# Optimization experiments

Measured on AMD Instinct MI355X. Metric: run time of the kernel, lower is better.

Reference implementation:

```python
import jax, jax.numpy as jnp
import numpy as np

B, N, DIM = 4, 4096, 1024
HEADS, DIM_HEAD = 16, 64
ATTN_SCALE = 8.0
EPS = 1e-12


def setup_inputs() -> dict:
    key = jax.random.key(0)
    k1, k2, k3 = jax.random.split(key, 3)
    dim_inner = HEADS * DIM_HEAD
    return {
        "x": jax.random.normal(k1, (B, N, DIM), dtype=jnp.float32),
        "gamma": jnp.ones((DIM,), dtype=jnp.float32),
        "w_qkv": jax.random.normal(k2, (3 * dim_inner, DIM), dtype=jnp.float32) * 0.02,
        "temperature": jnp.ones((HEADS, 1, 1), dtype=jnp.float32),
        "w_out": jax.random.normal(k3, (DIM, dim_inner), dtype=jnp.float32) * 0.02,
    }


def _l2norm(t, axis=-1):
    # matches F.normalize: x / max(||x||, eps)
    n = jnp.sqrt(jnp.sum(t * t, axis=axis, keepdims=True))
    return t / jnp.maximum(n, EPS)


def reference(x, gamma, w_qkv, temperature, w_out):
    b, n, dim = x.shape
    h, dh = HEADS, DIM_HEAD
    # RMSNorm: F.normalize(x, dim=-1) * sqrt(dim) * gamma
    xn = _l2norm(x) * jnp.sqrt(jnp.float32(dim)) * gamma
    # QKV projection, rearrange 'b n (qkv h d) -> qkv b h d n'
    qkv = jnp.einsum('bnc,oc->bno', xn, w_qkv)
    qkv = qkv.reshape(b, n, 3, h, dh).transpose(2, 0, 3, 4, 1)  # (3, b, h, dh, n)
    q, k, v = qkv[0], qkv[1], qkv[2]
    # l2-normalize along n (last axis), learned per-head temperature on q
    q = _l2norm(q) * jnp.exp(temperature)
    k = _l2norm(k)
    # cross-covariance attention over feature dim: scores are (b,h,dh,dh)
    sim = jnp.einsum('bhdn,bhen->bhde', q, k) * ATTN_SCALE
    attn = jax.nn.softmax(sim, axis=-1)
    out = jnp.einsum('bhde,bhen->bhdn', attn, v)
    # rearrange 'b h d n -> b n (h d)' and output projection
    out = out.transpose(0, 3, 1, 2).reshape(b, n, h * dh)
    return jnp.einsum('bni,oi->bno', out, w_out)
```

## Files before the change

### kernel.cpp

```cpp
#include <hip/hip_runtime.h>
#include <hip/hip_bf16.h>
#include <cstdint>
#include <cstddef>

#define BB    4
#define NN    4096
#define DIM   1024
#define HEADS 16
#define DH    64
#define DIN   1024
#define NQO   3072
#define MTOT  (BB*NN)
#define KDIM  1024
#define EPS_F 1e-12f

using bf16 = __hip_bfloat16;
typedef __attribute__((ext_vector_type(8))) short bf16x8;
typedef __attribute__((ext_vector_type(4))) float f32x4;

__device__ __forceinline__ void gload_lds16(const void* g, void* l) {
    __builtin_amdgcn_global_load_lds(
        (const __attribute__((address_space(1))) void*)g,
        (__attribute__((address_space(3))) void*)l,
        16, 0, 0);
}

__device__ __forceinline__ ushort bf16_bits(float x) {
    union { bf16 h; ushort u; } c;
    c.h = __float2bfloat16(x);
    return c.u;
}

__device__ __forceinline__ float b2f(ushort u) {
    union { unsigned u32; float f; } c;
    c.u32 = ((unsigned)u) << 16;
    return c.f;
}

__global__ __launch_bounds__(256) void k_rmsnorm(const float* __restrict__ x,
                                                 const float* __restrict__ gamma,
                                                 bf16* __restrict__ xn) {
    int row = blockIdx.x;
    int t = threadIdx.x;
    const float4* xr = (const float4*)(x + (size_t)row * DIM);
    float4 v = xr[t];
    float ss = v.x * v.x + v.y * v.y + v.z * v.z + v.w * v.w;
#pragma unroll
    for (int off = 32; off; off >>= 1) ss += __shfl_down(ss, off, 64);
    __shared__ float red[4];
    int lane = t & 63, w = t >> 6;
    if (lane == 0) red[w] = ss;
    __syncthreads();
    float tot = red[0] + red[1] + red[2] + red[3];
    float scale = 32.0f / fmaxf(sqrtf(tot), EPS_F);
    float4 g = ((const float4*)gamma)[t];
    union { ushort4 u4; ushort us[4]; } o;
    o.us[0] = bf16_bits(v.x * scale * g.x);
    o.us[1] = bf16_bits(v.y * scale * g.y);
    o.us[2] = bf16_bits(v.z * scale * g.z);
    o.us[3] = bf16_bits(v.w * scale * g.w);
    ((ushort4*)(xn + (size_t)row * DIM))[t] = o.u4;
}

__global__ __launch_bounds__(256) void k_cast_bf16(const float* __restrict__ s,
                                                   bf16* __restrict__ d, int n4) {
    int i = blockIdx.x * blockDim.x + threadIdx.x;
    if (i >= n4) return;
    float4 v = ((const float4*)s)[i];
    union { ushort4 u4; ushort us[4]; } o;
    o.us[0] = bf16_bits(v.x); o.us[1] = bf16_bits(v.y);
    o.us[2] = bf16_bits(v.z); o.us[3] = bf16_bits(v.w);
    ((ushort4*)d)[i] = o.u4;
}

__global__ __launch_bounds__(256, 2) void k_gemm_qkv(const bf16* __restrict__ A,
                                                     const bf16* __restrict__ W,
                                                     bf16* __restrict__ qkv) {
    __shared__ short As[128 * 32];
    __shared__ short Bs[128 * 32];
    const int tm = blockIdx.y * 128;
    const int tn = blockIdx.x * 128;
    const int t = threadIdx.x, lane = t & 63, w = t >> 6;
    const int wr = w >> 1, wc = w & 1;

    f32x4 acc[4][4] = {};

    const int ca = w * 2;
    const int rowS = ca * 16 + (lane >> 2);
    const int kofs = (lane & 3) * 8;
    const bf16* Ab = A + (size_t)(tm + rowS) * KDIM + kofs;
    const bf16* Bb = W + (size_t)(tn + rowS) * KDIM + kofs;
    short* AsD0 = As + ca * 512;
    short* AsD1 = As + (ca + 1) * 512;
    short* BsD0 = Bs + ca * 512;
    short* BsD1 = Bs + (ca + 1) * 512;

    const int rbA = wr * 64 + (lane & 15);
    const int rbB = wc * 64 + (lane & 15);
    const int kh = (lane >> 4) * 8;

    for (int kk = 0; kk < KDIM; kk += 32) {
        __syncthreads();
        gload_lds16(Ab + kk, AsD0);
        gload_lds16(Ab + kk + 16 * KDIM, AsD1);
        gload_lds16(Bb + kk, BsD0);
        gload_lds16(Bb + kk + 16 * KDIM, BsD1);
        __syncthreads();
        bf16x8 af[4], bfr[4];
#pragma unroll
        for (int i = 0; i < 4; ++i) {
            af[i]  = *(const bf16x8*)(As + (rbA + i * 16) * 32 + kh);
            bfr[i] = *(const bf16x8*)(Bs + (rbB + i * 16) * 32 + kh);
        }
#pragma unroll
        for (int i = 0; i < 4; ++i)
#pragma unroll
            for (int j = 0; j < 4; ++j)
                acc[i][j] = __builtin_amdgcn_mfma_f32_16x16x32_bf16(af[i], bfr[j], acc[i][j], 0, 0, 0);
    }

    const int b = tm >> 12;
#pragma unroll
    for (int i = 0; i < 4; ++i) {
        int mg = tm + wr * 64 + i * 16 + (lane >> 4) * 4;
        int nseq = mg & (NN - 1);
#pragma unroll
        for (int j = 0; j < 4; ++j) {
            int o = tn + wc * 64 + j * 16 + (lane & 15);
            size_t row = (size_t)((o >> 10) * 4 + b) * 1024 + (o & 1023);
            union { ushort4 u4; ushort us[4]; } pk;
#pragma unroll
            for (int r = 0; r < 4; ++r) pk.us[r] = bf16_bits(acc[i][j][r]);
            *(ushort4*)(qkv + row * NN + nseq) = pk.u4;
        }
    }
}

__global__ __launch_bounds__(256) void k_rownorm(const bf16* __restrict__ qkv,
                                                 float* __restrict__ inv) {
    int row = blockIdx.x;
    const short* p = (const short*)(qkv + (size_t)row * NN);
    int t = threadIdx.x;
    bf16x8 a = *(const bf16x8*)(p + t * 16);
    bf16x8 b = *(const bf16x8*)(p + t * 16 + 8);
    float ss = 0.f;
#pragma unroll
    for (int i = 0; i < 8; ++i) {
        float fa = b2f((ushort)a[i]), fb = b2f((ushort)b[i]);
        ss += fa * fa + fb * fb;
    }
#pragma unroll
    for (int off = 32; off; off >>= 1) ss += __shfl_down(ss, off, 64);
    __shared__ float red[4];
    int lane = t & 63, w = t >> 6;
    if (lane == 0) red[w] = ss;
    __syncthreads();
    if (t == 0) {
        float tot = red[0] + red[1] + red[2] + red[3];
        inv[row] = 1.0f / fmaxf(sqrtf(tot), EPS_F);
    }
}

__global__ __launch_bounds__(256) void k_sim(const bf16* __restrict__ qkv,
                                             float* __restrict__ part) {
    __shared__ short Qs[64 * 32];
    __shared__ short Ks[64 * 32];
    const int chunk = blockIdx.x;
    const int bh = blockIdx.y;
    const int t = threadIdx.x, lane = t & 63, w = t >> 6;
    const bf16* qb = qkv + (size_t)(bh * 64) * NN;
    const bf16* kb = qkv + (size_t)(4096 + bh * 64) * NN;

    const size_t gofs = (size_t)(t >> 2) * NN + (t & 3) * 8 + chunk * 1024;
    short* QsD = Qs + w * 512;
    short* KsD = Ks + w * 512;

    const int ra = (w * 16 + (lane & 15)) * 32 + (lane >> 4) * 8;
    const int kh = (lane >> 4) * 8;

    f32x4 acc[4] = {};
    for (int nt = 0; nt < 32; ++nt) {
        __syncthreads();
        gload_lds16(qb + gofs + nt * 32, QsD);
        gload_lds16(kb + gofs + nt * 32, KsD);
        __syncthreads();
        bf16x8 af = *(const bf16x8*)(Qs + ra);
#pragma unroll
        for (int j = 0; j < 4; ++j) {
            bf16x8 bfr = *(const bf16x8*)(Ks + (j * 16 + (lane & 15)) * 32 + kh);
            acc[j] = __builtin_amdgcn_mfma_f32_16x16x32_bf16(af, bfr, acc[j], 0, 0, 0);
        }
    }
    float* pb = part + (size_t)(bh * 4 + chunk) * 4096;
#pragma unroll
    for (int j = 0; j < 4; ++j) {
        int e = j * 16 + (lane & 15);
#pragma unroll
        for (int r = 0; r < 4; ++r) {
            int d = w * 16 + (lane >> 4) * 4 + r;
            pb[d * 64 + e] = acc[j][r];
        }
    }
}

__global__ __launch_bounds__(256) void k_softfin(const float* __restrict__ part,
                                                 const float* __restrict__ inv,
                                                 const float* __restrict__ temp,
                                                 float* __restrict__ attnT) {
    int bh = blockIdx.x;
    int t = threadIdx.x, lane = t & 63, w = t >> 6;
    int e = lane;
    float expT = __expf(temp[bh & (HEADS - 1)]);
    float ike = inv[4096 + bh * 64 + e] * 8.0f * expT;
    const float* pb = part + (size_t)bh * 4 * 4096;
#pragma unroll 4
    for (int dd = 0; dd < 16; ++dd) {
        int d = w * 16 + dd;
        float s = pb[d * 64 + e] + pb[4096 + d * 64 + e] +
                  pb[8192 + d * 64 + e] + pb[12288 + d * 64 + e];
        float logit = s * ike * inv[bh * 64 + d];
        float m = logit;
#pragma unroll
        for (int off = 32; off; off >>= 1) m = fmaxf(m, __shfl_xor(m, off, 64));
        float p = __expf(logit - m);
        float sum = p;
#pragma unroll
        for (int off = 32; off; off >>= 1) sum += __shfl_xor(sum, off, 64);
        attnT[(size_t)bh * 4096 + e * 64 + d] = p / sum;
    }
}

__global__ __launch_bounds__(256) void k_attnv(const bf16* __restrict__ qkv,
                                               const float* __restrict__ attnT,
                                               bf16* __restrict__ A2) {
    int nchunk = blockIdx.x;
    int bh = blockIdx.y;
    int dz = blockIdx.z;
    int t = threadIdx.x;
    int n = nchunk * 1024 + t * 4;
    const bf16* vb = qkv + (size_t)(8192 + bh * 64) * NN;
    const float* at = attnT + (size_t)bh * 4096 + dz * 32;
    float acc[32][4];
#pragma unroll
    for (int d = 0; d < 32; ++d)
#pragma unroll
        for (int r = 0; r < 4; ++r) acc[d][r] = 0.f;

    for (int e = 0; e < 64; ++e) {
        ushort4 vraw = *(const ushort4*)((const short*)vb + (size_t)e * NN + n);
        float v0 = b2f(vraw.x), v1 = b2f(vraw.y), v2 = b2f(vraw.z), v3 = b2f(vraw.w);
        const float* arow = at + e * 64;
#pragma unroll
        for (int d = 0; d < 32; ++d) {
            float a = arow[d];
            acc[d][0] = fmaf(a, v0, acc[d][0]);
            acc[d][1] = fmaf(a, v1, acc[d][1]);
            acc[d][2] = fmaf(a, v2, acc[d][2]);
            acc[d][3] = fmaf(a, v3, acc[d][3]);
        }
    }
    int b = bh >> 4, h = bh & 15;
#pragma unroll
    for (int r = 0; r < 4; ++r) {
        bf16* dst = A2 + (size_t)(b * NN + n + r) * DIN + h * 64 + dz * 32;
        alignas(16) ushort tmp[32];
#pragma unroll
        for (int d = 0; d < 32; ++d) tmp[d] = bf16_bits(acc[d][r]);
        uint4* d4 = (uint4*)dst;
        const uint4* s4 = (const uint4*)tmp;
        d4[0] = s4[0]; d4[1] = s4[1]; d4[2] = s4[2]; d4[3] = s4[3];
    }
}

__global__ __launch_bounds__(256, 2) void k_gemm_out(const bf16* __restrict__ A,
                                                     const bf16* __restrict__ W,
                                                     float* __restrict__ out) {
    __shared__ short As[128 * 32];
    __shared__ short Bs[128 * 32];
    const int tm = blockIdx.y * 128;
    const int tn = blockIdx.x * 128;
    const int t = threadIdx.x, lane = t & 63, w = t >> 6;
    const int wr = w >> 1, wc = w & 1;

    f32x4 acc[4][4] = {};

    const int ca = w * 2;
    const int rowS = ca * 16 + (lane >> 2);
    const int kofs = (lane & 3) * 8;
    const bf16* Ab = A + (size_t)(tm + rowS) * KDIM + kofs;
    const bf16* Bb = W + (size_t)(tn + rowS) * KDIM + kofs;
    short* AsD0 = As + ca * 512;
    short* AsD1 = As + (ca + 1) * 512;
    short* BsD0 = Bs + ca * 512;
    short* BsD1 = Bs + (ca + 1) * 512;

    const int rbA = wr * 64 + (lane & 15);
    const int rbB = wc * 64 + (lane & 15);
    const int kh = (lane >> 4) * 8;

    for (int kk = 0; kk < KDIM; kk += 32) {
        __syncthreads();
        gload_lds16(Ab + kk, AsD0);
        gload_lds16(Ab + kk + 16 * KDIM, AsD1);
        gload_lds16(Bb + kk, BsD0);
        gload_lds16(Bb + kk + 16 * KDIM, BsD1);
        __syncthreads();
        bf16x8 af[4], bfr[4];
#pragma unroll
        for (int i = 0; i < 4; ++i) {
            af[i]  = *(const bf16x8*)(As + (rbA + i * 16) * 32 + kh);
            bfr[i] = *(const bf16x8*)(Bs + (rbB + i * 16) * 32 + kh);
        }
#pragma unroll
        for (int i = 0; i < 4; ++i)
#pragma unroll
            for (int j = 0; j < 4; ++j)
                acc[i][j] = __builtin_amdgcn_mfma_f32_16x16x32_bf16(af[i], bfr[j], acc[i][j], 0, 0, 0);
    }

#pragma unroll
    for (int i = 0; i < 4; ++i) {
        int mg = tm + wr * 64 + i * 16 + (lane >> 4) * 4;
#pragma unroll
        for (int j = 0; j < 4; ++j) {
            int o = tn + wc * 64 + j * 16 + (lane & 15);
#pragma unroll
            for (int r = 0; r < 4; ++r)
                out[(size_t)(mg + r) * DIN + o] = acc[i][j][r];
        }
    }
}

extern "C" void kernel_launch(void* const* d_in, const int* in_sizes, int n_in,
                              void* d_out, int out_size, void* d_ws, size_t ws_size,
                              hipStream_t stream) {
    const float* x      = (const float*)d_in[0];
    const float* gamma  = (const float*)d_in[1];
    const float* w_qkv  = (const float*)d_in[2];
    const float* temp   = (const float*)d_in[3];
    const float* w_out  = (const float*)d_in[4];
    float* out = (float*)d_out;

    char* ws = (char*)d_ws;
    bf16*  qkv   = (bf16*)ws;
    bf16*  xn    = (bf16*)(ws + 100663296);
    bf16*  wq_bf = (bf16*)(ws + 134217728);
    bf16*  wo_bf = (bf16*)(ws + 140509184);
    float* inv   = (float*)(ws + 142606336);
    float* part  = (float*)(ws + 142639104);
    float* attnT = (float*)(ws + 146833408);

    k_rmsnorm<<<MTOT, 256, 0, stream>>>(x, gamma, xn);
    k_cast_bf16<<<(NQO * KDIM / 4 + 255) / 256, 256, 0, stream>>>(w_qkv, wq_bf, NQO * KDIM / 4);
    k_cast_bf16<<<(DIN * KDIM / 4 + 255) / 256, 256, 0, stream>>>(w_out, wo_bf, DIN * KDIM / 4);
    k_gemm_qkv<<<dim3(NQO / 128, MTOT / 128), 256, 0, stream>>>(xn, wq_bf, qkv);
    k_rownorm<<<8192, 256, 0, stream>>>(qkv, inv);
    k_sim<<<dim3(4, 64), 256, 0, stream>>>(qkv, part);
    k_softfin<<<64, 256, 0, stream>>>(part, inv, temp, attnT);
    bf16* A2 = xn;
    k_attnv<<<dim3(4, 64, 2), 256, 0, stream>>>(qkv, attnT, A2);
    k_gemm_out<<<dim3(DIN / 128, MTOT / 128), 256, 0, stream>>>(A2, wo_bf, out);
}
```

Measured before the change: 388.2 us.

## Fuse row norms into sim kernel and move attn@V onto MFMA with transposed V

Removes the separate row-norm kernel by accumulating q/k sum-of-squares inside the sim kernel via atomics, with a zeroing kernel added first. The sim kernel gets double-buffered swizzled LDS staging for K and doubles the chunk count. The QKV GEMM writes V in an (n, d) transposed layout so the attn@V step can run on bf16 MFMA, replacing the scalar FMA loop. Softmax weights are now stored as bf16 rather than fp32. In exchange, the transposed V stores are scattered 2-byte writes, the atomics add contention, and bf16 attention weights lose precision.

```diff
diff --git a/kernel.cpp b/kernel.cpp
--- a/kernel.cpp
+++ b/kernel.cpp
@@ -73,6 +73,11 @@
     ((ushort4*)d)[i] = o.u4;
 }
 
+__global__ __launch_bounds__(256) void k_zero(float* __restrict__ p, int n) {
+    int i = blockIdx.x * 256 + threadIdx.x;
+    if (i < n) p[i] = 0.0f;
+}
+
 __global__ __launch_bounds__(256, 2) void k_gemm_qkv(const bf16* __restrict__ A,
                                                      const bf16* __restrict__ W,
                                                      bf16* __restrict__ qkv) {
@@ -120,105 +125,133 @@
     }
 
     const int b = tm >> 12;
-#pragma unroll
-    for (int i = 0; i < 4; ++i) {
-        int mg = tm + wr * 64 + i * 16 + (lane >> 4) * 4;
-        int nseq = mg & (NN - 1);
-#pragma unroll
-        for (int j = 0; j < 4; ++j) {
-            int o = tn + wc * 64 + j * 16 + (lane & 15);
-            size_t row = (size_t)((o >> 10) * 4 + b) * 1024 + (o & 1023);
-            union { ushort4 u4; ushort us[4]; } pk;
-#pragma unroll
-            for (int r = 0; r < 4; ++r) pk.us[r] = bf16_bits(acc[i][j][r]);
-            *(ushort4*)(qkv + row * NN + nseq) = pk.u4;
-        }
-    }
-}
-
-__global__ __launch_bounds__(256) void k_rownorm(const bf16* __restrict__ qkv,
-                                                 float* __restrict__ inv) {
-    int row = blockIdx.x;
-    const short* p = (const short*)(qkv + (size_t)row * NN);
-    int t = threadIdx.x;
-    bf16x8 a = *(const bf16x8*)(p + t * 16);
-    bf16x8 b = *(const bf16x8*)(p + t * 16 + 8);
-    float ss = 0.f;
-#pragma unroll
-    for (int i = 0; i < 8; ++i) {
-        float fa = b2f((ushort)a[i]), fb = b2f((ushort)b[i]);
-        ss += fa * fa + fb * fb;
-    }
-#pragma unroll
-    for (int off = 32; off; off >>= 1) ss += __shfl_down(ss, off, 64);
-    __shared__ float red[4];
-    int lane = t & 63, w = t >> 6;
-    if (lane == 0) red[w] = ss;
-    __syncthreads();
-    if (t == 0) {
-        float tot = red[0] + red[1] + red[2] + red[3];
-        inv[row] = 1.0f / fmaxf(sqrtf(tot), EPS_F);
+    if (tn < 2048) {
+#pragma unroll
+        for (int i = 0; i < 4; ++i) {
+            int mg = tm + wr * 64 + i * 16 + ((lane >> 4) << 2);
+            int nseq = mg & (NN - 1);
+#pragma unroll
+            for (int j = 0; j < 4; ++j) {
+                int o = tn + wc * 64 + j * 16 + (lane & 15);
+                size_t row = (size_t)((o >> 10) * 4 + b) * 1024 + (o & 1023);
+                union { ushort4 u4; ushort us[4]; } pk;
+#pragma unroll
+                for (int r = 0; r < 4; ++r) pk.us[r] = bf16_bits(acc[i][j][r]);
+                *(ushort4*)(qkv + row * NN + nseq) = pk.u4;
+            }
+        }
+    } else {
+        bf16* vT = qkv + (size_t)8192 * NN;
+#pragma unroll
+        for (int i = 0; i < 4; ++i) {
+            int mg = tm + wr * 64 + i * 16 + ((lane >> 4) << 2);
+            int nseq = mg & (NN - 1);
+#pragma unroll
+            for (int j = 0; j < 4; ++j) {
+                int o = tn + wc * 64 + j * 16 + (lane & 15);
+                int hd = o & 1023;
+                size_t base = ((size_t)(b * 16 + (hd >> 6)) * NN + nseq) * 64 + (hd & 63);
+#pragma unroll
+                for (int r = 0; r < 4; ++r)
+                    vT[base + (size_t)r * 64] = __float2bfloat16(acc[i][j][r]);
+            }
+        }
     }
 }
 
 __global__ __launch_bounds__(256) void k_sim(const bf16* __restrict__ qkv,
-                                             float* __restrict__ part) {
-    __shared__ short Qs[64 * 32];
-    __shared__ short Ks[64 * 32];
+                                             float* __restrict__ part,
+                                             float* __restrict__ ss) {
+    __shared__ short Ks[2][8192];
     const int chunk = blockIdx.x;
     const int bh = blockIdx.y;
     const int t = threadIdx.x, lane = t & 63, w = t >> 6;
     const bf16* qb = qkv + (size_t)(bh * 64) * NN;
     const bf16* kb = qkv + (size_t)(4096 + bh * 64) * NN;
-
-    const size_t gofs = (size_t)(t >> 2) * NN + (t & 3) * 8 + chunk * 1024;
-    short* QsD = Qs + w * 512;
-    short* KsD = Ks + w * 512;
-
-    const int ra = (w * 16 + (lane & 15)) * 32 + (lane >> 4) * 8;
-    const int kh = (lane >> 4) * 8;
+    const int n0b = chunk * 512;
+
+#define SIM_STAGE(buf, nt) do {                                              \
+    int n0_ = n0b + (nt) * 128;                                              \
+    _Pragma("unroll")                                                        \
+    for (int cc = 0; cc < 4; ++cc) {                                         \
+        int row_ = cc * 16 + (t >> 4);                                       \
+        int colb_ = ((t & 15) << 4) ^ ((row_ & 7) << 4);                     \
+        gload_lds16(kb + (size_t)row_ * NN + n0_ + (colb_ >> 1),             \
+                    &Ks[buf][cc * 2048 + w * 512]);                          \
+    }                                                                        \
+} while (0)
 
     f32x4 acc[4] = {};
-    for (int nt = 0; nt < 32; ++nt) {
-        __syncthreads();
-        gload_lds16(qb + gofs + nt * 32, QsD);
-        gload_lds16(kb + gofs + nt * 32, KsD);
-        __syncthreads();
-        bf16x8 af = *(const bf16x8*)(Qs + ra);
-#pragma unroll
-        for (int j = 0; j < 4; ++j) {
-            bf16x8 bfr = *(const bf16x8*)(Ks + (j * 16 + (lane & 15)) * 32 + kh);
-            acc[j] = __builtin_amdgcn_mfma_f32_16x16x32_bf16(af, bfr, acc[j], 0, 0, 0);
-        }
-    }
-    float* pb = part + (size_t)(bh * 4 + chunk) * 4096;
+    float ssq = 0.f, ssk = 0.f;
+
+    SIM_STAGE(0, 0);
+    __syncthreads();
+    for (int nt = 0; nt < 4; ++nt) {
+        if (nt < 3) SIM_STAGE((nt + 1) & 1, nt + 1);
+        {
+            const int buf = nt & 1;
+            const int n0 = n0b + nt * 128;
+            bf16x8 af[4];
+#pragma unroll
+            for (int ks = 0; ks < 4; ++ks) {
+                af[ks] = *(const bf16x8*)(qb + (size_t)(w * 16 + (lane & 15)) * NN +
+                                          n0 + ks * 32 + ((lane >> 4) << 3));
+#pragma unroll
+                for (int i = 0; i < 8; ++i) { float f = b2f((ushort)af[ks][i]); ssq += f * f; }
+            }
+#pragma unroll
+            for (int j = 0; j < 4; ++j) {
+                int e = j * 16 + (lane & 15);
+#pragma unroll
+                for (int ks = 0; ks < 4; ++ks) {
+                    bf16x8 bfr = *(const bf16x8*)((const char*)&Ks[buf][0] + e * 256 +
+                                  ((ks * 64 + ((lane >> 4) << 4)) ^ ((e & 7) << 4)));
+                    if (j == w) {
+#pragma unroll
+                        for (int i = 0; i < 8; ++i) { float f = b2f((ushort)bfr[i]); ssk += f * f; }
+                    }
+                    acc[j] = __builtin_amdgcn_mfma_f32_16x16x32_bf16(af[ks], bfr, acc[j], 0, 0, 0);
+                }
+            }
+        }
+        __syncthreads();
+    }
+#undef SIM_STAGE
+
+    float vq = ssq; vq += __shfl_xor(vq, 16, 64); vq += __shfl_xor(vq, 32, 64);
+    if (lane < 16) atomicAdd(&ss[bh * 64 + w * 16 + lane], vq);
+    float vk = ssk; vk += __shfl_xor(vk, 16, 64); vk += __shfl_xor(vk, 32, 64);
+    if (lane < 16) atomicAdd(&ss[4096 + bh * 64 + w * 16 + lane], vk);
+
+    float* pb = part + (size_t)(bh * 8 + chunk) * 4096;
 #pragma unroll
     for (int j = 0; j < 4; ++j) {
         int e = j * 16 + (lane & 15);
 #pragma unroll
         for (int r = 0; r < 4; ++r) {
-            int d = w * 16 + (lane >> 4) * 4 + r;
+            int d = w * 16 + ((lane >> 4) << 2) + r;
             pb[d * 64 + e] = acc[j][r];
         }
     }
 }
 
 __global__ __launch_bounds__(256) void k_softfin(const float* __restrict__ part,
-                                                 const float* __restrict__ inv,
+                                                 const float* __restrict__ ss,
                                                  const float* __restrict__ temp,
-                                                 float* __restrict__ attnT) {
+                                                 bf16* __restrict__ attn) {
     int bh = blockIdx.x;
-    int t = threadIdx.x, lane = t & 63, w = t >> 6;
-    int e = lane;
+    int t = threadIdx.x, e = t & 63, w = t >> 6;
     float expT = __expf(temp[bh & (HEADS - 1)]);
-    float ike = inv[4096 + bh * 64 + e] * 8.0f * expT;
-    const float* pb = part + (size_t)bh * 4 * 4096;
-#pragma unroll 4
+    float ike = 8.0f * expT / fmaxf(sqrtf(ss[4096 + bh * 64 + e]), EPS_F);
+    const float* pb = part + (size_t)bh * 8 * 4096;
+#pragma unroll 2
     for (int dd = 0; dd < 16; ++dd) {
         int d = w * 16 + dd;
-        float s = pb[d * 64 + e] + pb[4096 + d * 64 + e] +
-                  pb[8192 + d * 64 + e] + pb[12288 + d * 64 + e];
-        float logit = s * ike * inv[bh * 64 + d];
+        float s = 0.f;
+#pragma unroll
+        for (int c = 0; c < 8; ++c) s += pb[c * 4096 + d * 64 + e];
+        float invq = 1.0f / fmaxf(sqrtf(ss[bh * 64 + d]), EPS_F);
+        float logit = s * ike * invq;
         float m = logit;
 #pragma unroll
         for (int off = 32; off; off >>= 1) m = fmaxf(m, __shfl_xor(m, off, 64));
@@ -226,50 +259,51 @@
         float sum = p;
 #pragma unroll
         for (int off = 32; off; off >>= 1) sum += __shfl_xor(sum, off, 64);
-        attnT[(size_t)bh * 4096 + e * 64 + d] = p / sum;
+        attn[(size_t)bh * 4096 + d * 64 + e] = __float2bfloat16(p / sum);
     }
 }
 
 __global__ __launch_bounds__(256) void k_attnv(const bf16* __restrict__ qkv,
-                                               const float* __restrict__ attnT,
+                                               const bf16* __restrict__ attn,
                                                bf16* __restrict__ A2) {
-    int nchunk = blockIdx.x;
-    int bh = blockIdx.y;
-    int dz = blockIdx.z;
-    int t = threadIdx.x;
-    int n = nchunk * 1024 + t * 4;
-    const bf16* vb = qkv + (size_t)(8192 + bh * 64) * NN;
-    const float* at = attnT + (size_t)bh * 4096 + dz * 32;
-    float acc[32][4];
-#pragma unroll
-    for (int d = 0; d < 32; ++d)
-#pragma unroll
-        for (int r = 0; r < 4; ++r) acc[d][r] = 0.f;
-
-    for (int e = 0; e < 64; ++e) {
-        ushort4 vraw = *(const ushort4*)((const short*)vb + (size_t)e * NN + n);
-        float v0 = b2f(vraw.x), v1 = b2f(vraw.y), v2 = b2f(vraw.z), v3 = b2f(vraw.w);
-        const float* arow = at + e * 64;
-#pragma unroll
-        for (int d = 0; d < 32; ++d) {
-            float a = arow[d];
-            acc[d][0] = fmaf(a, v0, acc[d][0]);
-            acc[d][1] = fmaf(a, v1, acc[d][1]);
-            acc[d][2] = fmaf(a, v2, acc[d][2]);
-            acc[d][3] = fmaf(a, v3, acc[d][3]);
-        }
-    }
-    int b = bh >> 4, h = bh & 15;
-#pragma unroll
-    for (int r = 0; r < 4; ++r) {
-        bf16* dst = A2 + (size_t)(b * NN + n + r) * DIN + h * 64 + dz * 32;
-        alignas(16) ushort tmp[32];
-#pragma unroll
-        for (int d = 0; d < 32; ++d) tmp[d] = bf16_bits(acc[d][r]);
-        uint4* d4 = (uint4*)dst;
-        const uint4* s4 = (const uint4*)tmp;
-        d4[0] = s4[0]; d4[1] = s4[1]; d4[2] = s4[2]; d4[3] = s4[3];
-    }
+    const int nc = blockIdx.x;
+    const int bh = blockIdx.y;
+    const int t = threadIdx.x, lane = t & 63, w = t >> 6;
+    const bf16* vT = qkv + (size_t)8192 * NN + (size_t)bh * NN * 64;
+    const bf16* ab = attn + (size_t)bh * 4096;
+    const int nbase = nc * 256 + w * 64;
+
+    bf16x8 bfr[4][2];
+#pragma unroll
+    for (int df = 0; df < 4; ++df)
+#pragma unroll
+        for (int ks = 0; ks < 2; ++ks)
+            bfr[df][ks] = *(const bf16x8*)(ab + (df * 16 + (lane & 15)) * 64 +
+                                           ks * 32 + ((lane >> 4) << 3));
+
+    f32x4 acc[4][4] = {};
+#pragma unroll
+    for (int nf = 0; nf < 4; ++nf) {
+#pragma unroll
+        for (int ks = 0; ks < 2; ++ks) {
+            bf16x8 af = *(const bf16x8*)(vT + (size_t)(nbase + nf * 16 + (lane & 15)) * 64 +
+                                         ks * 32 + ((lane >> 4) << 3));
+#pragma unroll
+            for (int df = 0; df < 4; ++df)
+                acc[nf][df] = __builtin_amdgcn_mfma_f32_16x16x32_bf16(af, bfr[df][ks], acc[nf][df], 0, 0, 0);
+        }
+    }
+    const int b = bh >> 4, h = bh & 15;
+#pragma unroll
+    for (int nf = 0; nf < 4; ++nf)
+#pragma unroll
+        for (int df = 0; df < 4; ++df)
+#pragma unroll
+            for (int r = 0; r < 4; ++r) {
+                int n = nbase + nf * 16 + ((lane >> 4) << 2) + r;
+                int d = df * 16 + (lane & 15);
+                A2[(size_t)(b * NN + n) * DIN + h * 64 + d] = __float2bfloat16(acc[nf][df][r]);
+            }
 }
 
 __global__ __launch_bounds__(256, 2) void k_gemm_out(const bf16* __restrict__ A,
@@ -342,22 +376,22 @@
     float* out = (float*)d_out;
 
     char* ws = (char*)d_ws;
-    bf16*  qkv   = (bf16*)ws;
-    bf16*  xn    = (bf16*)(ws + 100663296);
-    bf16*  wq_bf = (bf16*)(ws + 134217728);
-    bf16*  wo_bf = (bf16*)(ws + 140509184);
-    float* inv   = (float*)(ws + 142606336);
-    float* part  = (float*)(ws + 142639104);
-    float* attnT = (float*)(ws + 146833408);
+    bf16*  qkv    = (bf16*)ws;
+    bf16*  xn     = (bf16*)(ws + 100663296);
+    bf16*  wq_bf  = (bf16*)(ws + 134217728);
+    bf16*  wo_bf  = (bf16*)(ws + 140509184);
+    float* ss     = (float*)(ws + 142606336);
+    float* part   = (float*)(ws + 142639104);
+    bf16*  attnw  = (bf16*)(ws + 151027712);
 
     k_rmsnorm<<<MTOT, 256, 0, stream>>>(x, gamma, xn);
     k_cast_bf16<<<(NQO * KDIM / 4 + 255) / 256, 256, 0, stream>>>(w_qkv, wq_bf, NQO * KDIM / 4);
     k_cast_bf16<<<(DIN * KDIM / 4 + 255) / 256, 256, 0, stream>>>(w_out, wo_bf, DIN * KDIM / 4);
+    k_zero<<<32, 256, 0, stream>>>(ss, 8192);
     k_gemm_qkv<<<dim3(NQO / 128, MTOT / 128), 256, 0, stream>>>(xn, wq_bf, qkv);
-    k_rownorm<<<8192, 256, 0, stream>>>(qkv, inv);
-    k_sim<<<dim3(4, 64), 256, 0, stream>>>(qkv, part);
-    k_softfin<<<64, 256, 0, stream>>>(part, inv, temp, attnT);
+    k_sim<<<dim3(8, 64), 256, 0, stream>>>(qkv, part, ss);
+    k_softfin<<<64, 256, 0, stream>>>(part, ss, temp, attnw);
     bf16* A2 = xn;
-    k_attnv<<<dim3(4, 64, 2), 256, 0, stream>>>(qkv, attnT, A2);
+    k_attnv<<<dim3(16, 64), 256, 0, stream>>>(qkv, attnw, A2);
     k_gemm_out<<<dim3(DIN / 128, MTOT / 128), 256, 0, stream>>>(A2, wo_bf, out);
 }
```

After: 350.3 us. 9.8% less time.
